# Optimization experiments

Hardware: AMD Instinct MI355X
Metric: run time of the kernel (lower is better)

Reference implementation:

```python
import jax, jax.numpy as jnp
import numpy as np

B, SQ, SK, D, DV = 8, 2048, 4096, 512, 256

def setup_inputs() -> dict:
    key = jax.random.key(0)
    k1, k2, k3, k4, k5 = jax.random.split(key, 5)
    X = jax.random.normal(k1, (B, SQ, D), dtype=jnp.float32)
    Y = jax.random.normal(k2, (SK, D), dtype=jnp.float32)
    Z = jax.random.normal(k3, (SK, D), dtype=jnp.float32)
    # Linear weights (torch stores [out, in]); scaled like default init
    W_k = jax.random.normal(k4, (D, D), dtype=jnp.float32) / np.sqrt(D)
    W_v = jax.random.normal(k5, (DV, D), dtype=jnp.float32) / np.sqrt(D)
    return {"X": X, "Y": Y, "Z": Z, "W_k": W_k, "W_v": W_v, "rate": 0}


def reference(X, Y, Z, W_k, W_v, rate):
    # key = W_k(Y).unsqueeze(0): [1, SK, D]; value = W_v(Z).unsqueeze(0): [1, SK, DV]
    key = (Y @ W_k.T)[None]
    value = (Z @ W_v.T)[None]
    # scores = X @ key^T / sqrt(d): [B, SQ, SK] (key batch dim broadcasts)
    scale = 1.0 / jnp.sqrt(jnp.asarray(X.shape[-1], dtype=X.dtype))
    scores = jnp.matmul(X, jnp.swapaxes(key, 1, 2)) * scale
    attn = jax.nn.softmax(scores, axis=-1)
    # dropout layers act as identity in eval mode
    out = jnp.matmul(attn, value)  # [B, SQ, DV]
    return out
```

## Files before the change

kernel.cpp:

```cpp
#include <hip/hip_runtime.h>
#include <hip/hip_bf16.h>

#define NB    8
#define SQN   2048
#define SKN   4096
#define DDIM  512
#define DVDIM 256
#define NROWS (NB*SQN)
#define NS    2
#define NJ    ((SKN/64)/NS)

typedef __attribute__((ext_vector_type(8)))  short bf16x8;
typedef __attribute__((ext_vector_type(4)))  short bf16x4;
typedef __attribute__((ext_vector_type(4)))  float f32x4;
typedef __attribute__((ext_vector_type(16))) float f32x16;

__device__ __forceinline__ short f2bf(float f) {
    unsigned u = __float_as_uint(f);
    return (short)((u + 0x7FFFu + ((u >> 16) & 1u)) >> 16);
}

#define BAR_LGKM() do {                                                       \
    asm volatile("s_waitcnt lgkmcnt(0)" ::: "memory");                        \
    __builtin_amdgcn_sched_barrier(0);                                        \
    __builtin_amdgcn_s_barrier();                                             \
    __builtin_amdgcn_sched_barrier(0);                                        \
} while (0)

__global__ __launch_bounds__(256, 2) void proj_gemms(
    const float* __restrict__ Y, const float* __restrict__ Z,
    const float* __restrict__ Wk, const float* __restrict__ Wv,
    unsigned short* __restrict__ keyb, unsigned short* __restrict__ vtb)
{
    __shared__ short sA[64*128];
    __shared__ short sB[64*128];
    const float *A, *Bm;
    unsigned short* C;
    int m0, n0;
    const bool kpath = (blockIdx.z == 0);
    if (kpath) {
        A = Y; Bm = Wk; C = keyb;
        m0 = blockIdx.x * 64; n0 = blockIdx.y * 64;
    } else {
        int lin = blockIdx.x * 8 + blockIdx.y;
        if (lin >= 256) return;
        A = Wv; Bm = Z; C = vtb;
        m0 = (lin >> 6) * 64; n0 = (lin & 63) * 64;
    }
    const int tid  = threadIdx.x;
    const int wave = tid >> 6;
    const int lane = tid & 63;
    const int quad = lane >> 4;
    const int l15  = lane & 15;

    f32x4 acc[4];
    #pragma unroll
    for (int n = 0; n < 4; ++n) { acc[n][0]=0.f; acc[n][1]=0.f; acc[n][2]=0.f; acc[n][3]=0.f; }

    float4 ra[8], rb[8];
    #pragma unroll
    for (int it = 0; it < 8; ++it) {
        int f = it*1024 + tid*4, row = f >> 7, col = f & 127;
        ra[it] = *(const float4*)(A  + (size_t)(m0+row)*DDIM + col);
        rb[it] = *(const float4*)(Bm + (size_t)(n0+row)*DDIM + col);
    }

    for (int kc = 0; kc < DDIM; kc += 128) {
        __syncthreads();
        #pragma unroll
        for (int it = 0; it < 8; ++it) {
            int f = it*1024 + tid*4;
            bf16x4 a4; a4[0]=f2bf(ra[it].x); a4[1]=f2bf(ra[it].y); a4[2]=f2bf(ra[it].z); a4[3]=f2bf(ra[it].w);
            *(bf16x4*)(sA + f) = a4;
            bf16x4 b4; b4[0]=f2bf(rb[it].x); b4[1]=f2bf(rb[it].y); b4[2]=f2bf(rb[it].z); b4[3]=f2bf(rb[it].w);
            *(bf16x4*)(sB + f) = b4;
        }
        __syncthreads();
        if (kc + 128 < DDIM) {
            #pragma unroll
            for (int it = 0; it < 8; ++it) {
                int f = it*1024 + tid*4, row = f >> 7, col = f & 127;
                ra[it] = *(const float4*)(A  + (size_t)(m0+row)*DDIM + kc + 128 + col);
                rb[it] = *(const float4*)(Bm + (size_t)(n0+row)*DDIM + kc + 128 + col);
            }
        }
        #pragma unroll
        for (int t = 0; t < 4; ++t) {
            bf16x8 af = *(const bf16x8*)(sA + (wave*16 + l15)*128 + t*32 + quad*8);
            #pragma unroll
            for (int n = 0; n < 4; ++n) {
                bf16x8 bfr = *(const bf16x8*)(sB + (n*16 + l15)*128 + t*32 + quad*8);
                acc[n] = __builtin_amdgcn_mfma_f32_16x16x32_bf16(af, bfr, acc[n], 0, 0, 0);
            }
        }
    }
    #pragma unroll
    for (int n = 0; n < 4; ++n)
        #pragma unroll
        for (int r = 0; r < 4; ++r) {
            int m  = m0 + wave*16 + quad*4 + r;
            int nn = n0 + n*16 + l15;
            unsigned short v = (unsigned short)f2bf(acc[n][r]);
            size_t off;
            if (kpath) {
                int J = m >> 6, kh = (m >> 5) & 1, ls = m & 31;
                int c = nn >> 7, tp = (nn >> 4) & 7, hd = (nn >> 3) & 1, d7 = nn & 7;
                off = (size_t)(((J*4 + c)*8 + tp)*2 + kh)*512 + (hd*32 + ls)*8 + d7;
            } else {
                int J = nn >> 6, g = (nn >> 4) & 3, hk = (nn >> 3) & 1, k7 = nn & 7;
                int wv = m >> 7, n2 = (m >> 5) & 3, lv = m & 31;
                off = (size_t)((J*8 + wv*4 + n2)*4 + g)*512 + (hk*32 + lv)*8 + k7;
            }
            C[off] = v;
        }
}

__global__ __launch_bounds__(128, 2) void attn_fused(
    const float* __restrict__ X,
    const unsigned short* __restrict__ Kb,
    const unsigned short* __restrict__ Vt,
    float* __restrict__ Opart,
    float* __restrict__ Mpart,
    float* __restrict__ Lpart)
{
    __shared__ __align__(16) char smem[37376];
    char* sQ   = smem;
    char* sPex = smem + 32768;
    float* sSt = (float*)(smem + 36864);

    const int tid  = threadIdx.x;
    const int wk   = tid >> 6;
    const int lane = tid & 63;
    const int l31  = lane & 31;
    const int hi   = lane >> 5;

    const int bid   = blockIdx.x;
    const int xcd   = bid & 7;
    const int slot  = bid >> 3;
    const int split = xcd >> 2;
    const int q0    = ((xcd & 3)*128 + slot) * 32;
    const float scale = 0.04419417382415922f * 1.4426950408889634f;

    {
        const float* xrow = X + (size_t)(q0 + l31)*DDIM + hi*8;
        #pragma unroll
        for (int i = 0; i < 16; ++i) {
            const int t2 = wk*16 + i;
            float4 a = *(const float4*)(xrow + t2*16);
            float4 b = *(const float4*)(xrow + t2*16 + 4);
            bf16x8 q;
            q[0]=f2bf(a.x*scale); q[1]=f2bf(a.y*scale); q[2]=f2bf(a.z*scale); q[3]=f2bf(a.w*scale);
            q[4]=f2bf(b.x*scale); q[5]=f2bf(b.y*scale); q[6]=f2bf(b.z*scale); q[7]=f2bf(b.w*scale);
            *(bf16x8*)(sQ + t2*1024 + lane*16) = q;
        }
    }

    f32x16 o[4];
    #pragma unroll
    for (int n = 0; n < 4; ++n)
        #pragma unroll
        for (int r = 0; r < 16; ++r) o[n][r] = 0.f;
    float m_r = -1e30f, l_r = 0.f;

    const int Jg0 = split * NJ;
    const char* kp = (const char*)Kb + (size_t)Jg0*65536 + wk*1024 + lane*16;
    const char* vp = (const char*)Vt + (size_t)Jg0*32768 + wk*16384 + lane*16;
    #define KOFF(h_, t_) ((size_t)((h_)>>1)*16384 + (size_t)((((h_)&1)*4 + (t_))*2)*1024)

    bf16x8 kf[3][4];
    bf16x8 vf[2][4];

    BAR_LGKM();

    #pragma unroll
    for (int t = 0; t < 4; ++t) kf[0][t] = *(const bf16x8*)(kp + KOFF(0, t));
    #pragma unroll
    for (int t = 0; t < 4; ++t) kf[1][t] = *(const bf16x8*)(kp + KOFF(1, t));

    const char* qb = sQ + lane*16;

    for (int j = 0; j < NJ; ++j) {
        f32x16 s;
        #pragma unroll
        for (int r = 0; r < 16; ++r) s[r] = 0.f;

        #pragma unroll
        for (int h = 0; h < 8; ++h) {
            if (h < 6) {
                #pragma unroll
                for (int t = 0; t < 4; ++t)
                    kf[(h + 2) % 3][t] = *(const bf16x8*)(kp + KOFF(h + 2, t));
            } else {
                const int g = h - 6;
                #pragma unroll
                for (int n = 0; n < 4; ++n)
                    vf[g][n] = *(const bf16x8*)(vp + n*4096 + g*1024);
            }
            __builtin_amdgcn_s_setprio(1);
            #pragma unroll
            for (int t = 0; t < 4; ++t) {
                bf16x8 qv = *(const bf16x8*)(qb + (h*4 + t)*1024);
                s = __builtin_amdgcn_mfma_f32_32x32x16_bf16(
                        kf[h % 3][t], qv, s, 0, 0, 0);
            }
            __builtin_amdgcn_s_setprio(0);
        }

        float tmax = fmaxf(fmaxf(fmaxf(s[0],s[1]),fmaxf(s[2],s[3])),
                           fmaxf(fmaxf(s[4],s[5]),fmaxf(s[6],s[7])));
        tmax = fmaxf(tmax, fmaxf(fmaxf(fmaxf(s[8],s[9]),fmaxf(s[10],s[11])),
                                 fmaxf(fmaxf(s[12],s[13]),fmaxf(s[14],s[15]))));
        tmax = fmaxf(tmax, __shfl_xor(tmax, 32));
        if (lane < 32) sSt[(wk*2 + 0)*32 + lane] = tmax;
        BAR_LGKM();
        float tmax_o = sSt[((wk^1)*2 + 0)*32 + l31];
        const float tj   = fmaxf(tmax, tmax_o);
        const bool  upd  = tj > m_r + 8.0f;
        const float mn   = upd ? tj : m_r;
        float tsum = 0.f;
        #pragma unroll
        for (int r = 0; r < 16; ++r) { float pv = exp2f(s[r] - mn); s[r] = pv; tsum += pv; }
        tsum += __shfl_xor(tsum, 32);

        bf16x8 pf[2];
        #pragma unroll
        for (int ks = 0; ks < 2; ++ks) {
            int wA, wB, wC, wD;
            asm("v_cvt_pk_bf16_f32 %0, %1, %2" : "=v"(wA) : "v"(s[8*ks+0]), "v"(s[8*ks+1]));
            asm("v_cvt_pk_bf16_f32 %0, %1, %2" : "=v"(wB) : "v"(s[8*ks+2]), "v"(s[8*ks+3]));
            asm("v_cvt_pk_bf16_f32 %0, %1, %2" : "=v"(wC) : "v"(s[8*ks+4]), "v"(s[8*ks+5]));
            asm("v_cvt_pk_bf16_f32 %0, %1, %2" : "=v"(wD) : "v"(s[8*ks+6]), "v"(s[8*ks+7]));
            asm("v_permlane32_swap_b32 %0, %1" : "+v"(wA), "+v"(wC));
            asm("v_permlane32_swap_b32 %0, %1" : "+v"(wB), "+v"(wD));
            union { int w[4]; bf16x8 v; } u;
            u.w[0] = wA; u.w[1] = wB; u.w[2] = wC; u.w[3] = wD;
            pf[ks] = u.v;
        }
        *(bf16x8*)(sPex + (wk*2 + 0)*1024 + lane*16) = pf[0];
        *(bf16x8*)(sPex + (wk*2 + 1)*1024 + lane*16) = pf[1];
        if (lane < 32) sSt[(wk*2 + 1)*32 + lane] = tsum;

        if (j + 1 < NJ) {
            kp += 65536;
            #pragma unroll
            for (int t = 0; t < 4; ++t) kf[0][t] = *(const bf16x8*)(kp + KOFF(0, t));
            #pragma unroll
            for (int t = 0; t < 4; ++t) kf[1][t] = *(const bf16x8*)(kp + KOFF(1, t));
        }
        BAR_LGKM();
        float tsum_o = sSt[((wk^1)*2 + 1)*32 + l31];
        float alpha  = upd ? exp2f(m_r - mn) : 1.0f;
        l_r = l_r*alpha + (tsum + tsum_o);
        m_r = mn;
        if (__any(upd)) {
            #pragma unroll
            for (int r = 0; r < 16; ++r) {
                int row = (r&3) + 8*(r>>2) + 4*hi;
                float ar = __shfl(alpha, row);
                #pragma unroll
                for (int n = 0; n < 4; ++n) o[n][r] *= ar;
            }
        }

        const char* pb = sPex + lane*16;
        #pragma unroll
        for (int g = 0; g < 4; ++g) {
            bf16x8 pa = ((g >> 1) == wk) ? pf[g & 1]
                        : *(const bf16x8*)(pb + g*1024);
            __builtin_amdgcn_s_setprio(1);
            #pragma unroll
            for (int n = 0; n < 4; ++n)
                o[n] = __builtin_amdgcn_mfma_f32_32x32x16_bf16(
                        pa, vf[g & 1][n], o[n], 0, 0, 0);
            __builtin_amdgcn_s_setprio(0);
            if (g < 2) {
                #pragma unroll
                for (int n = 0; n < 4; ++n)
                    vf[g][n] = *(const bf16x8*)(vp + n*4096 + (g + 2)*1024);
            }
        }
        vp += 32768;
    }
    #undef KOFF

    const size_t base = (size_t)split * NROWS;
    if (wk == 0 && lane < 32) {
        Mpart[base + q0 + lane] = m_r;
        Lpart[base + q0 + lane] = l_r;
    }
    #pragma unroll
    for (int r = 0; r < 16; ++r) {
        int row = (r&3) + 8*(r>>2) + 4*hi;
        float* orow = Opart + (base + q0 + row) * (size_t)DVDIM + wk*128;
        #pragma unroll
        for (int n = 0; n < 4; ++n)
            orow[n*32 + l31] = o[n][r];
    }
}

__global__ void combine_splits(
    const float* __restrict__ Opart, const float* __restrict__ Mpart,
    const float* __restrict__ Lpart, float* __restrict__ out)
{
    const int row = blockIdx.x * 4 + (threadIdx.x >> 6);
    const int dv4 = (threadIdx.x & 63) * 4;
    float M = -1e30f;
    #pragma unroll
    for (int s = 0; s < NS; ++s) M = fmaxf(M, Mpart[(size_t)s*NROWS + row]);
    float denom = 0.f;
    float4 acc = make_float4(0.f, 0.f, 0.f, 0.f);
    #pragma unroll
    for (int s = 0; s < NS; ++s) {
        float w = exp2f(Mpart[(size_t)s*NROWS + row] - M);
        denom += Lpart[(size_t)s*NROWS + row] * w;
        float4 ov = *(const float4*)(Opart + ((size_t)s*NROWS + row)*DVDIM + dv4);
        acc.x += ov.x*w; acc.y += ov.y*w; acc.z += ov.z*w; acc.w += ov.w*w;
    }
    float inv = 1.0f / denom;
    *(float4*)(out + (size_t)row*DVDIM + dv4)
        = make_float4(acc.x*inv, acc.y*inv, acc.z*inv, acc.w*inv);
}

extern "C" void kernel_launch(void* const* d_in, const int* in_sizes, int n_in,
                              void* d_out, int out_size, void* d_ws, size_t ws_size,
                              hipStream_t stream) {
    const float* X  = (const float*)d_in[0];
    const float* Y  = (const float*)d_in[1];
    const float* Z  = (const float*)d_in[2];
    const float* Wk = (const float*)d_in[3];
    const float* Wv = (const float*)d_in[4];
    float* out = (float*)d_out;

    char* ws = (char*)d_ws;
    unsigned short* keyb = (unsigned short*)ws;
    unsigned short* vtb  = (unsigned short*)(ws + (4u<<20));
    float* Opart = (float*)(ws + (6u<<20));
    float* Mpart = (float*)(ws + (6u<<20) + (size_t)NS*NROWS*DVDIM*4);
    float* Lpart = Mpart + (size_t)NS*NROWS;

    proj_gemms<<<dim3(64, 8, 2), dim3(256), 0, stream>>>(Y, Z, Wk, Wv, keyb, vtb);
    attn_fused<<<dim3(1024), dim3(128), 0, stream>>>(
        X, keyb, vtb, Opart, Mpart, Lpart);
    combine_splits<<<dim3(NROWS/4), dim3(256), 0, stream>>>(Opart, Mpart, Lpart, out);
}
```

Before: 252.9 us.

## Process two 32-row query groups per block to reuse K/V fragments

Each attention block now handles 64 query rows (two 32-row groups) instead of 32, so each K and V fragment loaded from global memory feeds twice as many MFMAs. The grid is halved to 512 blocks, LDS doubles to about 73KB, and launch bounds drop to one block per CU hint to make room for the doubled accumulator and V fragment registers. The aim is to cut K/V global traffic per FLOP, at the cost of higher register pressure, lower occupancy and fewer blocks to fill the 256 CUs.

```diff
diff --git a/kernel.cpp b/kernel.cpp
--- a/kernel.cpp
+++ b/kernel.cpp
@@ -115,7 +115,7 @@
         }
 }
 
-__global__ __launch_bounds__(128, 2) void attn_fused(
+__global__ __launch_bounds__(128, 1) void attn_fused(
     const float* __restrict__ X,
     const unsigned short* __restrict__ Kb,
     const unsigned short* __restrict__ Vt,
@@ -123,10 +123,10 @@
     float* __restrict__ Mpart,
     float* __restrict__ Lpart)
 {
-    __shared__ __align__(16) char smem[37376];
+    __shared__ __align__(16) char smem[74752];
     char* sQ   = smem;
-    char* sPex = smem + 32768;
-    float* sSt = (float*)(smem + 36864);
+    char* sPex = smem + 65536;
+    float* sSt = (float*)(smem + 73728);
 
     const int tid  = threadIdx.x;
     const int wk   = tid >> 6;
@@ -138,29 +138,32 @@
     const int xcd   = bid & 7;
     const int slot  = bid >> 3;
     const int split = xcd >> 2;
-    const int q0    = ((xcd & 3)*128 + slot) * 32;
+    const int q0    = ((xcd & 3)*64 + slot) * 64;
     const float scale = 0.04419417382415922f * 1.4426950408889634f;
 
     {
-        const float* xrow = X + (size_t)(q0 + l31)*DDIM + hi*8;
-        #pragma unroll
-        for (int i = 0; i < 16; ++i) {
-            const int t2 = wk*16 + i;
+        const float* xrow = X + (size_t)(q0 + wk*32 + l31)*DDIM + hi*8;
+        char* qst = sQ + wk*32768;
+        #pragma unroll
+        for (int t2 = 0; t2 < 32; ++t2) {
             float4 a = *(const float4*)(xrow + t2*16);
             float4 b = *(const float4*)(xrow + t2*16 + 4);
             bf16x8 q;
             q[0]=f2bf(a.x*scale); q[1]=f2bf(a.y*scale); q[2]=f2bf(a.z*scale); q[3]=f2bf(a.w*scale);
             q[4]=f2bf(b.x*scale); q[5]=f2bf(b.y*scale); q[6]=f2bf(b.z*scale); q[7]=f2bf(b.w*scale);
-            *(bf16x8*)(sQ + t2*1024 + lane*16) = q;
-        }
-    }
-
-    f32x16 o[4];
-    #pragma unroll
-    for (int n = 0; n < 4; ++n)
-        #pragma unroll
-        for (int r = 0; r < 16; ++r) o[n][r] = 0.f;
-    float m_r = -1e30f, l_r = 0.f;
+            *(bf16x8*)(qst + t2*1024 + lane*16) = q;
+        }
+    }
+
+    f32x16 o[2][4];
+    #pragma unroll
+    for (int g2 = 0; g2 < 2; ++g2)
+        #pragma unroll
+        for (int n = 0; n < 4; ++n)
+            #pragma unroll
+            for (int r = 0; r < 16; ++r) o[g2][n][r] = 0.f;
+    float m_r[2] = {-1e30f, -1e30f};
+    float l_r[2] = {0.f, 0.f};
 
     const int Jg0 = split * NJ;
     const char* kp = (const char*)Kb + (size_t)Jg0*65536 + wk*1024 + lane*16;
@@ -168,7 +171,7 @@
     #define KOFF(h_, t_) ((size_t)((h_)>>1)*16384 + (size_t)((((h_)&1)*4 + (t_))*2)*1024)
 
     bf16x8 kf[3][4];
-    bf16x8 vf[2][4];
+    bf16x8 vf[4][4];
 
     BAR_LGKM();
 
@@ -180,9 +183,11 @@
     const char* qb = sQ + lane*16;
 
     for (int j = 0; j < NJ; ++j) {
-        f32x16 s;
-        #pragma unroll
-        for (int r = 0; r < 16; ++r) s[r] = 0.f;
+        f32x16 s[2];
+        #pragma unroll
+        for (int g2 = 0; g2 < 2; ++g2)
+            #pragma unroll
+            for (int r = 0; r < 16; ++r) s[g2][r] = 0.f;
 
         #pragma unroll
         for (int h = 0; h < 8; ++h) {
@@ -191,54 +196,75 @@
                 for (int t = 0; t < 4; ++t)
                     kf[(h + 2) % 3][t] = *(const bf16x8*)(kp + KOFF(h + 2, t));
             } else {
-                const int g = h - 6;
                 #pragma unroll
-                for (int n = 0; n < 4; ++n)
-                    vf[g][n] = *(const bf16x8*)(vp + n*4096 + g*1024);
+                for (int gg = 0; gg < 2; ++gg) {
+                    const int g = (h - 6)*2 + gg;
+                    #pragma unroll
+                    for (int n = 0; n < 4; ++n)
+                        vf[g][n] = *(const bf16x8*)(vp + n*4096 + g*1024);
+                }
             }
             __builtin_amdgcn_s_setprio(1);
             #pragma unroll
             for (int t = 0; t < 4; ++t) {
-                bf16x8 qv = *(const bf16x8*)(qb + (h*4 + t)*1024);
-                s = __builtin_amdgcn_mfma_f32_32x32x16_bf16(
-                        kf[h % 3][t], qv, s, 0, 0, 0);
+                #pragma unroll
+                for (int g2 = 0; g2 < 2; ++g2) {
+                    bf16x8 qv = *(const bf16x8*)(qb + g2*32768 + (h*4 + t)*1024);
+                    s[g2] = __builtin_amdgcn_mfma_f32_32x32x16_bf16(
+                            kf[h % 3][t], qv, s[g2], 0, 0, 0);
+                }
             }
             __builtin_amdgcn_s_setprio(0);
         }
 
-        float tmax = fmaxf(fmaxf(fmaxf(s[0],s[1]),fmaxf(s[2],s[3])),
-                           fmaxf(fmaxf(s[4],s[5]),fmaxf(s[6],s[7])));
-        tmax = fmaxf(tmax, fmaxf(fmaxf(fmaxf(s[8],s[9]),fmaxf(s[10],s[11])),
-                                 fmaxf(fmaxf(s[12],s[13]),fmaxf(s[14],s[15]))));
-        tmax = fmaxf(tmax, __shfl_xor(tmax, 32));
-        if (lane < 32) sSt[(wk*2 + 0)*32 + lane] = tmax;
+        float tmax[2];
+        #pragma unroll
+        for (int g2 = 0; g2 < 2; ++g2) {
+            float v = fmaxf(fmaxf(fmaxf(s[g2][0],s[g2][1]),fmaxf(s[g2][2],s[g2][3])),
+                            fmaxf(fmaxf(s[g2][4],s[g2][5]),fmaxf(s[g2][6],s[g2][7])));
+            v = fmaxf(v, fmaxf(fmaxf(fmaxf(s[g2][8],s[g2][9]),fmaxf(s[g2][10],s[g2][11])),
+                               fmaxf(fmaxf(s[g2][12],s[g2][13]),fmaxf(s[g2][14],s[g2][15]))));
+            v = fmaxf(v, __shfl_xor(v, 32));
+            tmax[g2] = v;
+            if (lane < 32) sSt[((wk*2 + g2)*2 + 0)*32 + lane] = v;
+        }
         BAR_LGKM();
-        float tmax_o = sSt[((wk^1)*2 + 0)*32 + l31];
-        const float tj   = fmaxf(tmax, tmax_o);
-        const bool  upd  = tj > m_r + 8.0f;
-        const float mn   = upd ? tj : m_r;
-        float tsum = 0.f;
-        #pragma unroll
-        for (int r = 0; r < 16; ++r) { float pv = exp2f(s[r] - mn); s[r] = pv; tsum += pv; }
-        tsum += __shfl_xor(tsum, 32);
-
-        bf16x8 pf[2];
-        #pragma unroll
-        for (int ks = 0; ks < 2; ++ks) {
-            int wA, wB, wC, wD;
-            asm("v_cvt_pk_bf16_f32 %0, %1, %2" : "=v"(wA) : "v"(s[8*ks+0]), "v"(s[8*ks+1]));
-            asm("v_cvt_pk_bf16_f32 %0, %1, %2" : "=v"(wB) : "v"(s[8*ks+2]), "v"(s[8*ks+3]));
-            asm("v_cvt_pk_bf16_f32 %0, %1, %2" : "=v"(wC) : "v"(s[8*ks+4]), "v"(s[8*ks+5]));
-            asm("v_cvt_pk_bf16_f32 %0, %1, %2" : "=v"(wD) : "v"(s[8*ks+6]), "v"(s[8*ks+7]));
-            asm("v_permlane32_swap_b32 %0, %1" : "+v"(wA), "+v"(wC));
-            asm("v_permlane32_swap_b32 %0, %1" : "+v"(wB), "+v"(wD));
-            union { int w[4]; bf16x8 v; } u;
-            u.w[0] = wA; u.w[1] = wB; u.w[2] = wC; u.w[3] = wD;
-            pf[ks] = u.v;
-        }
-        *(bf16x8*)(sPex + (wk*2 + 0)*1024 + lane*16) = pf[0];
-        *(bf16x8*)(sPex + (wk*2 + 1)*1024 + lane*16) = pf[1];
-        if (lane < 32) sSt[(wk*2 + 1)*32 + lane] = tsum;
+        bool  upd[2]; float mn[2], tsum[2];
+        #pragma unroll
+        for (int g2 = 0; g2 < 2; ++g2) {
+            float tmax_o = sSt[(((wk^1)*2 + g2)*2 + 0)*32 + l31];
+            float tj = fmaxf(tmax[g2], tmax_o);
+            upd[g2] = tj > m_r[g2] + 8.0f;
+            mn[g2]  = upd[g2] ? tj : m_r[g2];
+            float ts = 0.f;
+            #pragma unroll
+            for (int r = 0; r < 16; ++r) {
+                float pv = exp2f(s[g2][r] - mn[g2]); s[g2][r] = pv; ts += pv;
+            }
+            ts += __shfl_xor(ts, 32);
+            tsum[g2] = ts;
+        }
+
+        bf16x8 pf[2][2];
+        #pragma unroll
+        for (int g2 = 0; g2 < 2; ++g2)
+            #pragma unroll
+            for (int ks = 0; ks < 2; ++ks) {
+                int wA, wB, wC, wD;
+                asm("v_cvt_pk_bf16_f32 %0, %1, %2" : "=v"(wA) : "v"(s[g2][8*ks+0]), "v"(s[g2][8*ks+1]));
+                asm("v_cvt_pk_bf16_f32 %0, %1, %2" : "=v"(wB) : "v"(s[g2][8*ks+2]), "v"(s[g2][8*ks+3]));
+                asm("v_cvt_pk_bf16_f32 %0, %1, %2" : "=v"(wC) : "v"(s[g2][8*ks+4]), "v"(s[g2][8*ks+5]));
+                asm("v_cvt_pk_bf16_f32 %0, %1, %2" : "=v"(wD) : "v"(s[g2][8*ks+6]), "v"(s[g2][8*ks+7]));
+                asm("v_permlane32_swap_b32 %0, %1" : "+v"(wA), "+v"(wC));
+                asm("v_permlane32_swap_b32 %0, %1" : "+v"(wB), "+v"(wD));
+                union { int w[4]; bf16x8 v; } u;
+                u.w[0] = wA; u.w[1] = wB; u.w[2] = wC; u.w[3] = wD;
+                pf[g2][ks] = u.v;
+                *(bf16x8*)(sPex + (g2*4 + wk*2 + ks)*1024 + lane*16) = u.v;
+            }
+        #pragma unroll
+        for (int g2 = 0; g2 < 2; ++g2)
+            if (lane < 32) sSt[((wk*2 + g2)*2 + 1)*32 + lane] = tsum[g2];
 
         if (j + 1 < NJ) {
             kp += 65536;
@@ -248,53 +274,62 @@
             for (int t = 0; t < 4; ++t) kf[1][t] = *(const bf16x8*)(kp + KOFF(1, t));
         }
         BAR_LGKM();
-        float tsum_o = sSt[((wk^1)*2 + 1)*32 + l31];
-        float alpha  = upd ? exp2f(m_r - mn) : 1.0f;
-        l_r = l_r*alpha + (tsum + tsum_o);
-        m_r = mn;
-        if (__any(upd)) {
-            #pragma unroll
-            for (int r = 0; r < 16; ++r) {
-                int row = (r&3) + 8*(r>>2) + 4*hi;
-                float ar = __shfl(alpha, row);
+        int any_upd = 0;
+        #pragma unroll
+        for (int g2 = 0; g2 < 2; ++g2) {
+            float tsum_o = sSt[(((wk^1)*2 + g2)*2 + 1)*32 + l31];
+            float alpha  = upd[g2] ? exp2f(m_r[g2] - mn[g2]) : 1.0f;
+            l_r[g2] = l_r[g2]*alpha + (tsum[g2] + tsum_o);
+            m_r[g2] = mn[g2];
+            any_upd |= (int)upd[g2];
+            if (__any(upd[g2])) {
                 #pragma unroll
-                for (int n = 0; n < 4; ++n) o[n][r] *= ar;
+                for (int r = 0; r < 16; ++r) {
+                    int row = (r&3) + 8*(r>>2) + 4*hi;
+                    float ar = __shfl(alpha, row);
+                    #pragma unroll
+                    for (int n = 0; n < 4; ++n) o[g2][n][r] *= ar;
+                }
             }
         }
 
         const char* pb = sPex + lane*16;
+        __builtin_amdgcn_s_setprio(1);
         #pragma unroll
         for (int g = 0; g < 4; ++g) {
-            bf16x8 pa = ((g >> 1) == wk) ? pf[g & 1]
-                        : *(const bf16x8*)(pb + g*1024);
-            __builtin_amdgcn_s_setprio(1);
+            bf16x8 pa0 = ((g >> 1) == wk) ? pf[0][g & 1]
+                        : *(const bf16x8*)(pb + (0*4 + g)*1024);
+            bf16x8 pa1 = ((g >> 1) == wk) ? pf[1][g & 1]
+                        : *(const bf16x8*)(pb + (1*4 + g)*1024);
+            #pragma unroll
+            for (int n = 0; n < 4; ++n) {
+                o[0][n] = __builtin_amdgcn_mfma_f32_32x32x16_bf16(
+                        pa0, vf[g][n], o[0][n], 0, 0, 0);
+                o[1][n] = __builtin_amdgcn_mfma_f32_32x32x16_bf16(
+                        pa1, vf[g][n], o[1][n], 0, 0, 0);
+            }
+        }
+        __builtin_amdgcn_s_setprio(0);
+        vp += 32768;
+    }
+    #undef KOFF
+
+    const size_t base = (size_t)split * NROWS;
+    #pragma unroll
+    for (int g2 = 0; g2 < 2; ++g2) {
+        const int gr0 = q0 + g2*32;
+        if (wk == 0 && lane < 32) {
+            Mpart[base + gr0 + lane] = m_r[g2];
+            Lpart[base + gr0 + lane] = l_r[g2];
+        }
+        #pragma unroll
+        for (int r = 0; r < 16; ++r) {
+            int row = (r&3) + 8*(r>>2) + 4*hi;
+            float* orow = Opart + (base + gr0 + row) * (size_t)DVDIM + wk*128;
             #pragma unroll
             for (int n = 0; n < 4; ++n)
-                o[n] = __builtin_amdgcn_mfma_f32_32x32x16_bf16(
-                        pa, vf[g & 1][n], o[n], 0, 0, 0);
-            __builtin_amdgcn_s_setprio(0);
-            if (g < 2) {
-                #pragma unroll
-                for (int n = 0; n < 4; ++n)
-                    vf[g][n] = *(const bf16x8*)(vp + n*4096 + (g + 2)*1024);
-            }
-        }
-        vp += 32768;
-    }
-    #undef KOFF
-
-    const size_t base = (size_t)split * NROWS;
-    if (wk == 0 && lane < 32) {
-        Mpart[base + q0 + lane] = m_r;
-        Lpart[base + q0 + lane] = l_r;
-    }
-    #pragma unroll
-    for (int r = 0; r < 16; ++r) {
-        int row = (r&3) + 8*(r>>2) + 4*hi;
-        float* orow = Opart + (base + q0 + row) * (size_t)DVDIM + wk*128;
-        #pragma unroll
-        for (int n = 0; n < 4; ++n)
-            orow[n*32 + l31] = o[n][r];
+                orow[n*32 + l31] = o[g2][n][r];
+        }
     }
 }
 
@@ -339,7 +374,7 @@
     float* Lpart = Mpart + (size_t)NS*NROWS;
 
     proj_gemms<<<dim3(64, 8, 2), dim3(256), 0, stream>>>(Y, Z, Wk, Wv, keyb, vtb);
-    attn_fused<<<dim3(1024), dim3(128), 0, stream>>>(
+    attn_fused<<<dim3(512), dim3(128), 0, stream>>>(
         X, keyb, vtb, Opart, Mpart, Lpart);
     combine_splits<<<dim3(NROWS/4), dim3(256), 0, stream>>>(Opart, Mpart, Lpart, out);
 }
```

After: 249.8 us. No clear change (-1.2%).

## Make attention waves independent, each owning full key/value tiles for 32 rows

Applied to the files above, without the earlier changes.

Each wave now handles its own 32 query rows across all 64 keys and the full DV=256 output, instead of two waves splitting keys and value columns. This removes the per-iteration LDS exchange of row max, row sum and probabilities, along with both block barriers. The cost is doubled accumulator registers (8 output tiles), 64 KB of shared memory per block, occupancy dropped to one block per SIMD pair, and half as many blocks. Each wave also loads all of K and V for its tile, so per-wave global traffic doubles relative to its rows.

```diff
diff --git a/kernel.cpp b/kernel.cpp
--- a/kernel.cpp
+++ b/kernel.cpp
@@ -19,13 +19,6 @@
     unsigned u = __float_as_uint(f);
     return (short)((u + 0x7FFFu + ((u >> 16) & 1u)) >> 16);
 }
-
-#define BAR_LGKM() do {                                                       \
-    asm volatile("s_waitcnt lgkmcnt(0)" ::: "memory");                        \
-    __builtin_amdgcn_sched_barrier(0);                                        \
-    __builtin_amdgcn_s_barrier();                                             \
-    __builtin_amdgcn_sched_barrier(0);                                        \
-} while (0)
 
 __global__ __launch_bounds__(256, 2) void proj_gemms(
     const float* __restrict__ Y, const float* __restrict__ Z,
@@ -115,7 +108,7 @@
         }
 }
 
-__global__ __launch_bounds__(128, 2) void attn_fused(
+__global__ __launch_bounds__(128, 1) void attn_fused(
     const float* __restrict__ X,
     const unsigned short* __restrict__ Kb,
     const unsigned short* __restrict__ Vt,
@@ -123,13 +116,10 @@
     float* __restrict__ Mpart,
     float* __restrict__ Lpart)
 {
-    __shared__ __align__(16) char smem[37376];
-    char* sQ   = smem;
-    char* sPex = smem + 32768;
-    float* sSt = (float*)(smem + 36864);
+    __shared__ __align__(16) char smem[65536];
 
     const int tid  = threadIdx.x;
-    const int wk   = tid >> 6;
+    const int wave = tid >> 6;
     const int lane = tid & 63;
     const int l31  = lane & 31;
     const int hi   = lane >> 5;
@@ -138,162 +128,181 @@
     const int xcd   = bid & 7;
     const int slot  = bid >> 3;
     const int split = xcd >> 2;
-    const int q0    = ((xcd & 3)*128 + slot) * 32;
+    const int q0w   = ((xcd & 3)*64 + slot)*64 + wave*32;
     const float scale = 0.04419417382415922f * 1.4426950408889634f;
 
+    char* sQw = smem + wave*32768;
     {
-        const float* xrow = X + (size_t)(q0 + l31)*DDIM + hi*8;
-        #pragma unroll
-        for (int i = 0; i < 16; ++i) {
-            const int t2 = wk*16 + i;
+        const float* xrow = X + (size_t)(q0w + l31)*DDIM + hi*8;
+        #pragma unroll
+        for (int t2 = 0; t2 < 32; ++t2) {
             float4 a = *(const float4*)(xrow + t2*16);
             float4 b = *(const float4*)(xrow + t2*16 + 4);
             bf16x8 q;
             q[0]=f2bf(a.x*scale); q[1]=f2bf(a.y*scale); q[2]=f2bf(a.z*scale); q[3]=f2bf(a.w*scale);
             q[4]=f2bf(b.x*scale); q[5]=f2bf(b.y*scale); q[6]=f2bf(b.z*scale); q[7]=f2bf(b.w*scale);
-            *(bf16x8*)(sQ + t2*1024 + lane*16) = q;
-        }
-    }
-
-    f32x16 o[4];
-    #pragma unroll
-    for (int n = 0; n < 4; ++n)
+            *(bf16x8*)(sQw + t2*1024 + lane*16) = q;
+        }
+    }
+
+    f32x16 o[8];
+    #pragma unroll
+    for (int n = 0; n < 8; ++n)
         #pragma unroll
         for (int r = 0; r < 16; ++r) o[n][r] = 0.f;
     float m_r = -1e30f, l_r = 0.f;
 
-    const int Jg0 = split * NJ;
-    const char* kp = (const char*)Kb + (size_t)Jg0*65536 + wk*1024 + lane*16;
-    const char* vp = (const char*)Vt + (size_t)Jg0*32768 + wk*16384 + lane*16;
-    #define KOFF(h_, t_) ((size_t)((h_)>>1)*16384 + (size_t)((((h_)&1)*4 + (t_))*2)*1024)
-
-    bf16x8 kf[3][4];
-    bf16x8 vf[2][4];
-
-    BAR_LGKM();
-
-    #pragma unroll
-    for (int t = 0; t < 4; ++t) kf[0][t] = *(const bf16x8*)(kp + KOFF(0, t));
-    #pragma unroll
-    for (int t = 0; t < 4; ++t) kf[1][t] = *(const bf16x8*)(kp + KOFF(1, t));
-
-    const char* qb = sQ + lane*16;
+    const char* kp = (const char*)Kb + (size_t)split*NJ*65536 + lane*16;
+    const char* vp = (const char*)Vt + (size_t)split*NJ*32768 + lane*16;
+
+    bf16x8 kf[4][4];
+    bf16x8 vf[2][8];
+
+    #define LD_KS(bank_, boff_)                                               \
+        do { _Pragma("unroll")                                                \
+             for (int tt_ = 0; tt_ < 2; ++tt_)                                \
+                 _Pragma("unroll")                                            \
+                 for (int kh_ = 0; kh_ < 2; ++kh_)                            \
+                     kf[bank_][tt_*2 + kh_] = *(const bf16x8*)(kp + (boff_)   \
+                         + tt_*2048 + kh_*1024);                              \
+        } while (0)
+
+    #define LD_VG(bank_, g_)                                                  \
+        do { _Pragma("unroll")                                                \
+             for (int n_ = 0; n_ < 8; ++n_)                                   \
+                 vf[bank_][n_] = *(const bf16x8*)(vp + (n_>>2)*16384          \
+                     + (n_&3)*4096 + (g_)*1024);                              \
+        } while (0)
+
+    const char* qb = sQw + lane*16;
+
+    LD_KS(0, 0); LD_KS(1, 4096); LD_KS(2, 8192);
 
     for (int j = 0; j < NJ; ++j) {
-        f32x16 s;
-        #pragma unroll
-        for (int r = 0; r < 16; ++r) s[r] = 0.f;
-
-        #pragma unroll
-        for (int h = 0; h < 8; ++h) {
-            if (h < 6) {
-                #pragma unroll
-                for (int t = 0; t < 4; ++t)
-                    kf[(h + 2) % 3][t] = *(const bf16x8*)(kp + KOFF(h + 2, t));
-            } else {
-                const int g = h - 6;
-                #pragma unroll
-                for (int n = 0; n < 4; ++n)
-                    vf[g][n] = *(const bf16x8*)(vp + n*4096 + g*1024);
-            }
+        const bool hasN = (j + 1 < NJ);
+        f32x16 sc0, sc1;
+        #pragma unroll
+        for (int r = 0; r < 16; ++r) { sc0[r] = 0.f; sc1[r] = 0.f; }
+
+        #pragma unroll
+        for (int st = 0; st < 16; ++st) {
+            if (st < 13)       LD_KS((st + 3) & 3, (st + 3)*4096);
+            else if (st == 13) LD_VG(0, 0);
+            else if (st == 14) LD_VG(1, 1);
+            else if (hasN)     LD_KS(0, 65536);
             __builtin_amdgcn_s_setprio(1);
+            {
+                bf16x8 qa = *(const bf16x8*)(qb + (st*2 + 0)*1024);
+                bf16x8 qc = *(const bf16x8*)(qb + (st*2 + 1)*1024);
+                sc0 = __builtin_amdgcn_mfma_f32_32x32x16_bf16(kf[st & 3][0], qa, sc0, 0, 0, 0);
+                sc1 = __builtin_amdgcn_mfma_f32_32x32x16_bf16(kf[st & 3][1], qa, sc1, 0, 0, 0);
+                sc0 = __builtin_amdgcn_mfma_f32_32x32x16_bf16(kf[st & 3][2], qc, sc0, 0, 0, 0);
+                sc1 = __builtin_amdgcn_mfma_f32_32x32x16_bf16(kf[st & 3][3], qc, sc1, 0, 0, 0);
+            }
+            __builtin_amdgcn_s_setprio(0);
+        }
+
+        float tmax;
+        {
+            float v = fmaxf(fmaxf(fmaxf(sc0[0],sc0[1]),fmaxf(sc0[2],sc0[3])),
+                            fmaxf(fmaxf(sc0[4],sc0[5]),fmaxf(sc0[6],sc0[7])));
+            v = fmaxf(v, fmaxf(fmaxf(fmaxf(sc0[8],sc0[9]),fmaxf(sc0[10],sc0[11])),
+                               fmaxf(fmaxf(sc0[12],sc0[13]),fmaxf(sc0[14],sc0[15]))));
+            float w = fmaxf(fmaxf(fmaxf(sc1[0],sc1[1]),fmaxf(sc1[2],sc1[3])),
+                            fmaxf(fmaxf(sc1[4],sc1[5]),fmaxf(sc1[6],sc1[7])));
+            w = fmaxf(w, fmaxf(fmaxf(fmaxf(sc1[8],sc1[9]),fmaxf(sc1[10],sc1[11])),
+                               fmaxf(fmaxf(sc1[12],sc1[13]),fmaxf(sc1[14],sc1[15]))));
+            v = fmaxf(v, w);
+            v = fmaxf(v, __shfl_xor(v, 32));
+            tmax = v;
+        }
+        const bool  upd   = tmax > m_r + 8.0f;
+        const float mn    = upd ? tmax : m_r;
+        const float alpha = upd ? exp2f(m_r - mn) : 1.0f;
+        float tsum = 0.f;
+        #pragma unroll
+        for (int r = 0; r < 16; ++r) { float pv = exp2f(sc0[r] - mn); sc0[r] = pv; tsum += pv; }
+        #pragma unroll
+        for (int r = 0; r < 16; ++r) { float pv = exp2f(sc1[r] - mn); sc1[r] = pv; tsum += pv; }
+        tsum += __shfl_xor(tsum, 32);
+        l_r = l_r*alpha + tsum;
+        m_r = mn;
+
+        bf16x8 pf[4];
+        #pragma unroll
+        for (int kh = 0; kh < 2; ++kh) {
             #pragma unroll
-            for (int t = 0; t < 4; ++t) {
-                bf16x8 qv = *(const bf16x8*)(qb + (h*4 + t)*1024);
-                s = __builtin_amdgcn_mfma_f32_32x32x16_bf16(
-                        kf[h % 3][t], qv, s, 0, 0, 0);
-            }
-            __builtin_amdgcn_s_setprio(0);
-        }
-
-        float tmax = fmaxf(fmaxf(fmaxf(s[0],s[1]),fmaxf(s[2],s[3])),
-                           fmaxf(fmaxf(s[4],s[5]),fmaxf(s[6],s[7])));
-        tmax = fmaxf(tmax, fmaxf(fmaxf(fmaxf(s[8],s[9]),fmaxf(s[10],s[11])),
-                                 fmaxf(fmaxf(s[12],s[13]),fmaxf(s[14],s[15]))));
-        tmax = fmaxf(tmax, __shfl_xor(tmax, 32));
-        if (lane < 32) sSt[(wk*2 + 0)*32 + lane] = tmax;
-        BAR_LGKM();
-        float tmax_o = sSt[((wk^1)*2 + 0)*32 + l31];
-        const float tj   = fmaxf(tmax, tmax_o);
-        const bool  upd  = tj > m_r + 8.0f;
-        const float mn   = upd ? tj : m_r;
-        float tsum = 0.f;
-        #pragma unroll
-        for (int r = 0; r < 16; ++r) { float pv = exp2f(s[r] - mn); s[r] = pv; tsum += pv; }
-        tsum += __shfl_xor(tsum, 32);
-
-        bf16x8 pf[2];
-        #pragma unroll
-        for (int ks = 0; ks < 2; ++ks) {
-            int wA, wB, wC, wD;
-            asm("v_cvt_pk_bf16_f32 %0, %1, %2" : "=v"(wA) : "v"(s[8*ks+0]), "v"(s[8*ks+1]));
-            asm("v_cvt_pk_bf16_f32 %0, %1, %2" : "=v"(wB) : "v"(s[8*ks+2]), "v"(s[8*ks+3]));
-            asm("v_cvt_pk_bf16_f32 %0, %1, %2" : "=v"(wC) : "v"(s[8*ks+4]), "v"(s[8*ks+5]));
-            asm("v_cvt_pk_bf16_f32 %0, %1, %2" : "=v"(wD) : "v"(s[8*ks+6]), "v"(s[8*ks+7]));
-            asm("v_permlane32_swap_b32 %0, %1" : "+v"(wA), "+v"(wC));
-            asm("v_permlane32_swap_b32 %0, %1" : "+v"(wB), "+v"(wD));
-            union { int w[4]; bf16x8 v; } u;
-            u.w[0] = wA; u.w[1] = wB; u.w[2] = wC; u.w[3] = wD;
-            pf[ks] = u.v;
-        }
-        *(bf16x8*)(sPex + (wk*2 + 0)*1024 + lane*16) = pf[0];
-        *(bf16x8*)(sPex + (wk*2 + 1)*1024 + lane*16) = pf[1];
-        if (lane < 32) sSt[(wk*2 + 1)*32 + lane] = tsum;
-
-        if (j + 1 < NJ) {
-            kp += 65536;
-            #pragma unroll
-            for (int t = 0; t < 4; ++t) kf[0][t] = *(const bf16x8*)(kp + KOFF(0, t));
-            #pragma unroll
-            for (int t = 0; t < 4; ++t) kf[1][t] = *(const bf16x8*)(kp + KOFF(1, t));
-        }
-        BAR_LGKM();
-        float tsum_o = sSt[((wk^1)*2 + 1)*32 + l31];
-        float alpha  = upd ? exp2f(m_r - mn) : 1.0f;
-        l_r = l_r*alpha + (tsum + tsum_o);
-        m_r = mn;
+            for (int ks = 0; ks < 2; ++ks) {
+                int wA, wB, wC, wD;
+                if (kh == 0) {
+                    asm("v_cvt_pk_bf16_f32 %0, %1, %2" : "=v"(wA) : "v"(sc0[8*ks+0]), "v"(sc0[8*ks+1]));
+                    asm("v_cvt_pk_bf16_f32 %0, %1, %2" : "=v"(wB) : "v"(sc0[8*ks+2]), "v"(sc0[8*ks+3]));
+                    asm("v_cvt_pk_bf16_f32 %0, %1, %2" : "=v"(wC) : "v"(sc0[8*ks+4]), "v"(sc0[8*ks+5]));
+                    asm("v_cvt_pk_bf16_f32 %0, %1, %2" : "=v"(wD) : "v"(sc0[8*ks+6]), "v"(sc0[8*ks+7]));
+                } else {
+                    asm("v_cvt_pk_bf16_f32 %0, %1, %2" : "=v"(wA) : "v"(sc1[8*ks+0]), "v"(sc1[8*ks+1]));
+                    asm("v_cvt_pk_bf16_f32 %0, %1, %2" : "=v"(wB) : "v"(sc1[8*ks+2]), "v"(sc1[8*ks+3]));
+                    asm("v_cvt_pk_bf16_f32 %0, %1, %2" : "=v"(wC) : "v"(sc1[8*ks+4]), "v"(sc1[8*ks+5]));
+                    asm("v_cvt_pk_bf16_f32 %0, %1, %2" : "=v"(wD) : "v"(sc1[8*ks+6]), "v"(sc1[8*ks+7]));
+                }
+                asm("v_permlane32_swap_b32 %0, %1" : "+v"(wA), "+v"(wC));
+                asm("v_permlane32_swap_b32 %0, %1" : "+v"(wB), "+v"(wD));
+                union { int w[4]; bf16x8 v; } u;
+                u.w[0] = wA; u.w[1] = wB; u.w[2] = wC; u.w[3] = wD;
+                pf[kh*2 + ks] = u.v;
+            }
+        }
+
         if (__any(upd)) {
             #pragma unroll
             for (int r = 0; r < 16; ++r) {
                 int row = (r&3) + 8*(r>>2) + 4*hi;
                 float ar = __shfl(alpha, row);
                 #pragma unroll
-                for (int n = 0; n < 4; ++n) o[n][r] *= ar;
-            }
-        }
-
-        const char* pb = sPex + lane*16;
-        #pragma unroll
-        for (int g = 0; g < 4; ++g) {
-            bf16x8 pa = ((g >> 1) == wk) ? pf[g & 1]
-                        : *(const bf16x8*)(pb + g*1024);
-            __builtin_amdgcn_s_setprio(1);
-            #pragma unroll
-            for (int n = 0; n < 4; ++n)
-                o[n] = __builtin_amdgcn_mfma_f32_32x32x16_bf16(
-                        pa, vf[g & 1][n], o[n], 0, 0, 0);
-            __builtin_amdgcn_s_setprio(0);
-            if (g < 2) {
-                #pragma unroll
-                for (int n = 0; n < 4; ++n)
-                    vf[g][n] = *(const bf16x8*)(vp + n*4096 + (g + 2)*1024);
-            }
-        }
+                for (int n = 0; n < 8; ++n) o[n][r] *= ar;
+            }
+        }
+
+        __builtin_amdgcn_s_setprio(1);
+        #pragma unroll
+        for (int n = 0; n < 8; ++n)
+            o[n] = __builtin_amdgcn_mfma_f32_32x32x16_bf16(pf[0], vf[0][n], o[n], 0, 0, 0);
+        __builtin_amdgcn_s_setprio(0);
+        LD_VG(0, 2);
+        if (hasN) LD_KS(1, 65536 + 4096);
+        __builtin_amdgcn_s_setprio(1);
+        #pragma unroll
+        for (int n = 0; n < 8; ++n)
+            o[n] = __builtin_amdgcn_mfma_f32_32x32x16_bf16(pf[1], vf[1][n], o[n], 0, 0, 0);
+        __builtin_amdgcn_s_setprio(0);
+        LD_VG(1, 3);
+        if (hasN) LD_KS(2, 65536 + 8192);
+        __builtin_amdgcn_s_setprio(1);
+        #pragma unroll
+        for (int n = 0; n < 8; ++n)
+            o[n] = __builtin_amdgcn_mfma_f32_32x32x16_bf16(pf[2], vf[0][n], o[n], 0, 0, 0);
+        #pragma unroll
+        for (int n = 0; n < 8; ++n)
+            o[n] = __builtin_amdgcn_mfma_f32_32x32x16_bf16(pf[3], vf[1][n], o[n], 0, 0, 0);
+        __builtin_amdgcn_s_setprio(0);
+
+        kp += 65536;
         vp += 32768;
     }
-    #undef KOFF
+    #undef LD_KS
+    #undef LD_VG
 
     const size_t base = (size_t)split * NROWS;
-    if (wk == 0 && lane < 32) {
-        Mpart[base + q0 + lane] = m_r;
-        Lpart[base + q0 + lane] = l_r;
+    if (lane < 32) {
+        Mpart[base + q0w + lane] = m_r;
+        Lpart[base + q0w + lane] = l_r;
     }
     #pragma unroll
     for (int r = 0; r < 16; ++r) {
         int row = (r&3) + 8*(r>>2) + 4*hi;
-        float* orow = Opart + (base + q0 + row) * (size_t)DVDIM + wk*128;
-        #pragma unroll
-        for (int n = 0; n < 4; ++n)
+        float* orow = Opart + (base + q0w + row) * (size_t)DVDIM;
+        #pragma unroll
+        for (int n = 0; n < 8; ++n)
             orow[n*32 + l31] = o[n][r];
     }
 }
@@ -339,7 +348,7 @@
     float* Lpart = Mpart + (size_t)NS*NROWS;
 
     proj_gemms<<<dim3(64, 8, 2), dim3(256), 0, stream>>>(Y, Z, Wk, Wv, keyb, vtb);
-    attn_fused<<<dim3(1024), dim3(128), 0, stream>>>(
+    attn_fused<<<dim3(512), dim3(128), 0, stream>>>(
         X, keyb, vtb, Opart, Mpart, Lpart);
     combine_splits<<<dim3(NROWS/4), dim3(256), 0, stream>>>(Opart, Mpart, Lpart, out);
 }
```

Result: slower. 376.2 us (+48.8%).
